# Kernel tuning notes

Measured on AMD Instinct MI355X. Metric: run time of the kernel, lower is better.

The kernel has to match this reference:

```python
import jax, jax.numpy as jnp
import numpy as np
import math

D, H, S, B, E, FF = 768, 12, 1024, 2, 32768, 4 * 768
HD = D // H


def layer_norm(x, g, b, eps=1e-5):
    m = jnp.mean(x, axis=-1, keepdims=True)
    v = jnp.mean((x - m) ** 2, axis=-1, keepdims=True)
    return (x - m) / jnp.sqrt(v + eps) * g + b


def setup_inputs() -> dict:
    key = jax.random.key(0)
    ks = jax.random.split(key, 24)
    w = lambda k, shape: jax.random.normal(k, shape, dtype=jnp.float32) * 0.02
    inp = {
        "x": jax.random.normal(ks[0], (B, S, D), dtype=jnp.float32),
        "adj_mask": jax.random.randint(ks[1], (B, S, S), 0, 2).astype(bool),
        "edge_attr": jax.random.normal(ks[2], (E,), dtype=jnp.float32),
        "edge_index": jax.random.randint(ks[3], (2, E), 0, S),
        "norm1_g": jnp.ones((D,), jnp.float32),
        "norm1_b": jnp.zeros((D,), jnp.float32),
        "Wq": w(ks[4], (D, D)), "bq": jnp.zeros((D,), jnp.float32),
        "Wk": w(ks[5], (D, D)), "bk": jnp.zeros((D,), jnp.float32),
        "Wv": w(ks[6], (D, D)), "bv": jnp.zeros((D,), jnp.float32),
        "Wo": w(ks[7], (D, D)), "bo": jnp.zeros((D,), jnp.float32),
        "norm2_g": jnp.ones((D,), jnp.float32),
        "norm2_b": jnp.zeros((D,), jnp.float32),
        "mlp_W1": w(ks[8], (D, FF)), "mlp_b1": jnp.zeros((FF,), jnp.float32),
        "mlp_W2": w(ks[9], (FF, D)), "mlp_b2": jnp.zeros((D,), jnp.float32),
        # per-head edge-attr MLP: Linear(1,16) -> GELU -> Linear(16,1), stacked over H heads
        "ep_W1": w(ks[10], (H, 16)), "ep_b1": jnp.zeros((H, 16), jnp.float32),
        "ep_W2": w(ks[11], (H, 16)), "ep_b2": jnp.zeros((H,), jnp.float32),
    }
    return inp


def reference(x, adj_mask, edge_attr, edge_index,
              norm1_g, norm1_b, Wq, bq, Wk, bk, Wv, bv, Wo, bo,
              norm2_g, norm2_b, mlp_W1, mlp_b1, mlp_W2, mlp_b2,
              ep_W1, ep_b1, ep_W2, ep_b2):
    Bb, Ss, Dd = x.shape
    Hh = ep_W1.shape[0]
    hd = Dd // Hh
    residual = x
    nx = layer_norm(x, norm1_g, norm1_b)
    q = (nx @ Wq + bq).reshape(Bb, Ss, Hh, hd).transpose(0, 2, 1, 3)  # [B,H,S,hd]
    k = (nx @ Wk + bk).reshape(Bb, Ss, Hh, hd).transpose(0, 2, 1, 3)
    v = (nx @ Wv + bv).reshape(Bb, Ss, Hh, hd).transpose(0, 2, 1, 3)
    scores = jnp.einsum('bhqd,bhkd->bhqk', q, k) / math.sqrt(hd)
    mask = adj_mask.astype(bool)[:, None]  # [B,1,S,S]
    scores = jnp.where(mask, scores, jnp.float32(-1e9))
    # per-edge per-head bias (computed under no_grad in the original -> stop_gradient)
    h1 = jax.nn.gelu(edge_attr[:, None, None] * ep_W1[None] + ep_b1[None], approximate=False)  # [E,H,16]
    proj = jnp.einsum('ehk,hk->eh', h1, ep_W2) + ep_b2  # [E,H]
    proj = jax.lax.stop_gradient(proj)
    src, dst = edge_index[0], edge_index[1]
    bias = jnp.zeros((Hh, Ss, Ss), x.dtype).at[:, src, dst].set(proj.T)  # [H,S,S]
    scores = scores + jnp.where(mask, bias[None], jnp.float32(0.0))
    attn = jax.nn.softmax(scores, axis=-1)
    out = jnp.einsum('bhqk,bhkd->bhqd', attn, v)
    out = out.transpose(0, 2, 1, 3).reshape(Bb, Ss, Dd)
    x = residual + (out @ Wo + bo)
    y = layer_norm(x, norm2_g, norm2_b)
    y = jax.nn.gelu(y @ mlp_W1 + mlp_b1, approximate=False) @ mlp_W2 + mlp_b2
    return x + y
```

## Files before the change

### kernel.cpp

```cpp
#include <hip/hip_runtime.h>
#include <hip/hip_bf16.h>

#define B_ 2
#define S_ 1024
#define D_ 768
#define H_ 12
#define HD_ 64
#define FF_ 3072
#define E_ 32768
#define QS_ 2304
#define NSPLIT 4
#define NSPLIT_W2 4
#define BHS (B_ * H_ * S_)

typedef short bf16x8 __attribute__((ext_vector_type(8)));
typedef float f32x4 __attribute__((ext_vector_type(4)));

#define SW(row, seg) ((((seg) ^ ((row) & 7)) * 8))

__device__ __forceinline__ unsigned short f2bf(float f) {
    __hip_bfloat16 h = __float2bfloat16(f);
    return __builtin_bit_cast(unsigned short, h);
}
__device__ __forceinline__ float bf2f(unsigned short u) {
    unsigned int v = ((unsigned int)u) << 16;
    return __builtin_bit_cast(float, v);
}
__device__ __forceinline__ float gelu_exact(float x) {
    return 0.5f * x * (1.0f + erff(x * 0.70710678118654752f));
}
__device__ __forceinline__ void gload_lds16(const unsigned short* g, unsigned short* l) {
    __builtin_amdgcn_global_load_lds((const __attribute__((address_space(1))) void*)g,
                                     (__attribute__((address_space(3))) void*)l, 16, 0, 0);
}

__global__ __launch_bounds__(256) void prep_kernel(
    const void* __restrict__ adj, unsigned int* __restrict__ mp, int* __restrict__ winner,
    const float* __restrict__ Wq, const float* __restrict__ Wk, const float* __restrict__ Wv,
    const float* __restrict__ Wo, const float* __restrict__ W1, const float* __restrict__ W2,
    unsigned short* __restrict__ wqkvt, unsigned short* __restrict__ wot,
    unsigned short* __restrict__ w1t, unsigned short* __restrict__ w2t,
    const float* __restrict__ bq, const float* __restrict__ bk, const float* __restrict__ bv,
    float* __restrict__ bqkv,
    const float* __restrict__ x, const float* __restrict__ g1, const float* __restrict__ bn1,
    unsigned short* __restrict__ nxb)
{
    __shared__ float tile[32][33];
    __shared__ unsigned int words[32];
    __shared__ int u8f;
    __shared__ float red[8];
    const int blk = blockIdx.x;
    const int t = threadIdx.x;

    if (blk < 2048) {
        const int b = blk >> 10, q = blk & 1023;
        if (b == 0) {
            int4 v; v.x = -1; v.y = -1; v.z = -1; v.w = -1;
            reinterpret_cast<int4*>(winner)[q * 256 + t] = v;
        }
        if (t < 32) words[t] = 0;
        if (t == 0) u8f = 0;
        __syncthreads();
        const unsigned int* row8 = (const unsigned int*)((const unsigned char*)adj + ((size_t)b * S_ + q) * S_);
        const unsigned int* row32 = (const unsigned int*)((const int*)adj + ((size_t)b * S_ + q) * S_);
        const unsigned int v = row8[t];
        if (v & 0xFF00FF00u) atomicOr(&u8f, 1);
        __syncthreads();
        if (u8f) {
            unsigned int nib = 0;
            if (v & 0x000000FFu) nib |= 1u;
            if (v & 0x0000FF00u) nib |= 2u;
            if (v & 0x00FF0000u) nib |= 4u;
            if (v & 0xFF000000u) nib |= 8u;
            if (nib) atomicOr(&words[t >> 3], nib << ((t & 7) * 4));
        } else {
            for (int i = 0; i < 4; i++) {
                const int k = i * 256 + t;
                if (row32[k]) atomicOr(&words[k >> 5], 1u << (k & 31));
            }
        }
        __syncthreads();
        if (t < 32) mp[((size_t)b * S_ + q) * 32 + t] = words[t];
    } else if (blk < 8960) {
        const int w = blk - 2048;
        const float* src; unsigned short* dst; int K, N, nb, kb;
        if (w < 2304) {
            const int z = w / 576, r = w - z * 576;
            K = 768; N = 768; kb = (r / 24) * 32; nb = (r % 24) * 32;
            src = (z == 0) ? Wq : (z == 1) ? Wk : (z == 2) ? Wv : Wo;
            dst = (z == 3) ? wot : wqkvt + (size_t)z * 768 * 768;
        } else if (w < 4608) {
            const int r = w - 2304;
            K = 768; N = 3072; nb = (r % 96) * 32; kb = (r / 96) * 32;
            src = W1; dst = w1t;
        } else {
            const int r = w - 4608;
            K = 3072; N = 768; kb = (r % 96) * 32; nb = (r / 96) * 32;
            src = W2; dst = w2t;
        }
        const int tx = t & 31, ty = t >> 5;
        for (int r = 0; r < 32; r += 8)
            tile[ty + r][tx] = src[(size_t)(kb + ty + r) * N + nb + tx];
        __syncthreads();
        for (int r = 0; r < 32; r += 8)
            dst[(size_t)(nb + ty + r) * K + kb + tx] = f2bf(tile[tx][ty + r]);
        if (w == 0) {
            for (int i = t; i < QS_; i += 256)
                bqkv[i] = (i < 768) ? bq[i] : (i < 1536) ? bk[i - 768] : bv[i - 1536];
        }
    } else {
        const int row = blk - 8960;
        const float* xr = x + (size_t)row * D_;
        float v0 = xr[t], v1 = xr[t + 256], v2 = xr[t + 512];
        float s = v0 + v1 + v2, s2 = v0 * v0 + v1 * v1 + v2 * v2;
        for (int m = 32; m; m >>= 1) { s += __shfl_xor(s, m); s2 += __shfl_xor(s2, m); }
        const int w = t >> 6;
        if ((t & 63) == 0) { red[w] = s; red[4 + w] = s2; }
        __syncthreads();
        s = red[0] + red[1] + red[2] + red[3];
        s2 = red[4] + red[5] + red[6] + red[7];
        const float mean = s * (1.f / D_);
        const float var = s2 * (1.f / D_) - mean * mean;
        const float rstd = rsqrtf(var + 1e-5f);
        unsigned short* orow = nxb + (size_t)row * D_;
        orow[t]       = f2bf((v0 - mean) * rstd * g1[t]       + bn1[t]);
        orow[t + 256] = f2bf((v1 - mean) * rstd * g1[t + 256] + bn1[t + 256]);
        orow[t + 512] = f2bf((v2 - mean) * rstd * g1[t + 512] + bn1[t + 512]);
    }
}

__global__ __launch_bounds__(256) void ln_kernel(
    const float* __restrict__ x, const float* __restrict__ g,
    const float* __restrict__ b, unsigned short* __restrict__ out)
{
    const int row = blockIdx.x;
    const int t = threadIdx.x;
    const float* xr = x + (size_t)row * D_;
    float v0 = xr[t], v1 = xr[t + 256], v2 = xr[t + 512];
    float s = v0 + v1 + v2, s2 = v0 * v0 + v1 * v1 + v2 * v2;
    for (int m = 32; m; m >>= 1) { s += __shfl_xor(s, m); s2 += __shfl_xor(s2, m); }
    __shared__ float red[8];
    const int w = t >> 6;
    if ((t & 63) == 0) { red[w] = s; red[4 + w] = s2; }
    __syncthreads();
    s = red[0] + red[1] + red[2] + red[3];
    s2 = red[4] + red[5] + red[6] + red[7];
    const float mean = s * (1.f / D_);
    const float var = s2 * (1.f / D_) - mean * mean;
    const float rstd = rsqrtf(var + 1e-5f);
    unsigned short* orow = out + (size_t)row * D_;
    orow[t]       = f2bf((v0 - mean) * rstd * g[t]       + b[t]);
    orow[t + 256] = f2bf((v1 - mean) * rstd * g[t + 256] + b[t + 256]);
    orow[t + 512] = f2bf((v2 - mean) * rstd * g[t + 512] + b[t + 512]);
}

__global__ __launch_bounds__(256) void edge_proj_scatter_kernel(
    const float* __restrict__ ea, const float* __restrict__ W1, const float* __restrict__ b1,
    const float* __restrict__ W2, const float* __restrict__ b2,
    const int* __restrict__ ei, float* __restrict__ proj, int* __restrict__ winner)
{
    const int tid = blockIdx.x * 256 + threadIdx.x;
    const int e = tid / H_, h = tid - e * H_;
    const float a = ea[e];
    float s = 0.f;
    for (int j = 0; j < 16; j++) {
        const float tv = a * W1[h * 16 + j] + b1[h * 16 + j];
        s += gelu_exact(tv) * W2[h * 16 + j];
    }
    proj[tid] = s + b2[h];
    if (h == 0) {
        const int sn = ei[e], dn = ei[E_ + e];
        atomicMax(&winner[sn * S_ + dn], e);
    }
}

__global__ __launch_bounds__(256) void mid_kernel(
    const unsigned short* __restrict__ qkv, unsigned short* __restrict__ vt,
    const int* __restrict__ winner, const float* __restrict__ proj,
    unsigned short* __restrict__ ebias)
{
    __shared__ unsigned short T[64][68];
    const int blk = blockIdx.x;
    const int t = threadIdx.x;
    if (blk < 384) {
        const int s0 = (blk & 15) * 64;
        const int rest = blk >> 4;
        const int h = rest % 12, b = rest / 12;
        const int r = t >> 2, seg = t & 3;
        const unsigned short* src = qkv + (size_t)(b * S_ + s0 + r) * QS_ + 1536 + h * HD_ + seg * 16;
        *reinterpret_cast<uint4*>(&T[r][seg * 16])     = *reinterpret_cast<const uint4*>(src);
        *reinterpret_cast<uint4*>(&T[r][seg * 16 + 8]) = *reinterpret_cast<const uint4*>(src + 8);
        __syncthreads();
        unsigned short tmp[16];
        for (int i = 0; i < 16; i++) tmp[i] = T[seg * 16 + i][r];
        unsigned short* dst = vt + ((size_t)(b * H_ + h) * HD_ + r) * S_ + s0 + seg * 16;
        *reinterpret_cast<uint4*>(dst)     = *reinterpret_cast<uint4*>(&tmp[0]);
        *reinterpret_cast<uint4*>(dst + 8) = *reinterpret_cast<uint4*>(&tmp[8]);
    } else {
        const int q = blk - 384;
        const int k4 = t * 4;
        const int4 wv = *reinterpret_cast<const int4*>(&winner[q * S_ + k4]);
        for (int h = 0; h < H_; h++) {
            unsigned int lo = 0, hi = 0;
            if (wv.x >= 0) lo |= (unsigned int)f2bf(proj[(size_t)wv.x * H_ + h]);
            if (wv.y >= 0) lo |= ((unsigned int)f2bf(proj[(size_t)wv.y * H_ + h])) << 16;
            if (wv.z >= 0) hi |= (unsigned int)f2bf(proj[(size_t)wv.z * H_ + h]);
            if (wv.w >= 0) hi |= ((unsigned int)f2bf(proj[(size_t)wv.w * H_ + h])) << 16;
            uint2 val; val.x = lo; val.y = hi;
            *reinterpret_cast<uint2*>(&ebias[((size_t)h * S_ + q) * S_ + k4]) = val;
        }
    }
}

template<bool RES, bool OUTBF>
__global__ __launch_bounds__(256) void gemm_kernel(
    const unsigned short* __restrict__ A, const unsigned short* __restrict__ Bt,
    const float* __restrict__ bias, const float* __restrict__ res,
    void* __restrict__ outp, int M, int N, int K)
{
    __shared__ unsigned short As[64][40];
    __shared__ unsigned short Bs[64][40];
    const int m0 = blockIdx.y * 64, n0 = blockIdx.x * 64;
    const int t = threadIdx.x;
    const int w = t >> 6, l = t & 63;
    const int wm = w >> 1, wn = w & 1;
    const int r = l & 15, g = l >> 4;
    const int srow = t >> 2, sseg = t & 3;
    f32x4 acc[2][2] = {};
    for (int k0 = 0; k0 < K; k0 += 32) {
        __syncthreads();
        const uint4 av = *reinterpret_cast<const uint4*>(A + (size_t)(m0 + srow) * K + k0 + sseg * 8);
        *reinterpret_cast<uint4*>(&As[srow][sseg * 8]) = av;
        const uint4 bv = *reinterpret_cast<const uint4*>(Bt + (size_t)(n0 + srow) * K + k0 + sseg * 8);
        *reinterpret_cast<uint4*>(&Bs[srow][sseg * 8]) = bv;
        __syncthreads();
        bf16x8 af[2], bfr[2];
        af[0]  = *reinterpret_cast<const bf16x8*>(&As[wm * 32 + r][g * 8]);
        af[1]  = *reinterpret_cast<const bf16x8*>(&As[wm * 32 + 16 + r][g * 8]);
        bfr[0] = *reinterpret_cast<const bf16x8*>(&Bs[wn * 32 + r][g * 8]);
        bfr[1] = *reinterpret_cast<const bf16x8*>(&Bs[wn * 32 + 16 + r][g * 8]);
        for (int m = 0; m < 2; m++)
            for (int n = 0; n < 2; n++)
                acc[m][n] = __builtin_amdgcn_mfma_f32_16x16x32_bf16(af[m], bfr[n], acc[m][n], 0, 0, 0);
    }
    for (int m = 0; m < 2; m++)
        for (int n = 0; n < 2; n++) {
            const int col = n0 + wn * 32 + n * 16 + r;
            const float bvv = bias[col];
            for (int j = 0; j < 4; j++) {
                const int row = m0 + wm * 32 + m * 16 + g * 4 + j;
                float v = acc[m][n][j] + bvv;
                if (RES) v += res[(size_t)row * N + col];
                if (OUTBF) ((unsigned short*)outp)[(size_t)row * N + col] = f2bf(v);
                else       ((float*)outp)[(size_t)row * N + col] = v;
            }
        }
}

template<bool GELU, bool OUTBF, bool SPLITK>
__global__ __launch_bounds__(256) void gemm128_kernel(
    const unsigned short* __restrict__ A, const unsigned short* __restrict__ Bt,
    const float* __restrict__ bias, void* __restrict__ outp,
    int M, int N, int K, int klen, int scale_below)
{
    __shared__ unsigned short As[128][64];
    __shared__ unsigned short Bs[128][64];
    const int m0 = blockIdx.y * 128, n0 = blockIdx.x * 128;
    const int t = threadIdx.x;
    const int w = t >> 6, l = t & 63;
    const int wm = w >> 1, wn = w & 1;
    const int lr = l & 15, g = l >> 4;
    const int lrow8 = l >> 3;
    const int lseg = (l & 7) ^ lrow8;
    const int kbeg = SPLITK ? blockIdx.z * klen : 0;
    const int kend = SPLITK ? kbeg + klen : K;
    f32x4 acc[4][4] = {};
    for (int k0 = kbeg; k0 < kend; k0 += 64) {
        __syncthreads();
        for (int j = 0; j < 4; j++) {
            const int q = w * 4 + j;
            const int row = q * 8 + lrow8;
            gload_lds16(A  + (size_t)(m0 + row) * K + k0 + lseg * 8, &As[q * 8][0]);
            gload_lds16(Bt + (size_t)(n0 + row) * K + k0 + lseg * 8, &Bs[q * 8][0]);
        }
        __syncthreads();
        for (int kk = 0; kk < 2; kk++) {
            bf16x8 af[4], bfr[4];
            for (int m = 0; m < 4; m++) {
                const int r = wm * 64 + m * 16 + lr;
                af[m] = *reinterpret_cast<const bf16x8*>(&As[r][SW(r, kk * 4 + g)]);
            }
            for (int n = 0; n < 4; n++) {
                const int r = wn * 64 + n * 16 + lr;
                bfr[n] = *reinterpret_cast<const bf16x8*>(&Bs[r][SW(r, kk * 4 + g)]);
            }
            for (int m = 0; m < 4; m++)
                for (int n = 0; n < 4; n++)
                    acc[m][n] = __builtin_amdgcn_mfma_f32_16x16x32_bf16(af[m], bfr[n], acc[m][n], 0, 0, 0);
        }
    }
    if (SPLITK) {
        for (int m = 0; m < 4; m++)
            for (int n = 0; n < 4; n++) {
                const int col = n0 + wn * 64 + n * 16 + lr;
                for (int j = 0; j < 4; j++) {
                    const int row = m0 + wm * 64 + m * 16 + g * 4 + j;
                    if (OUTBF) ((unsigned short*)outp)[((size_t)blockIdx.z * M + row) * N + col] = f2bf(acc[m][n][j]);
                    else       ((float*)outp)[((size_t)blockIdx.z * M + row) * N + col] = acc[m][n][j];
                }
            }
    } else {
        for (int m = 0; m < 4; m++)
            for (int n = 0; n < 4; n++) {
                const int col = n0 + wn * 64 + n * 16 + lr;
                const float scl = (col < scale_below) ? 0.125f : 1.0f;
                const float bvv = bias[col];
                for (int j = 0; j < 4; j++) {
                    const int row = m0 + wm * 64 + m * 16 + g * 4 + j;
                    float v = (acc[m][n][j] + bvv) * scl;
                    if (GELU) v = gelu_exact(v);
                    if (OUTBF) ((unsigned short*)outp)[(size_t)row * N + col] = f2bf(v);
                    else       ((float*)outp)[(size_t)row * N + col] = v;
                }
            }
    }
}

__global__ __launch_bounds__(256) void w2_reduce_kernel(
    const unsigned short* __restrict__ part, const float* __restrict__ x2,
    const float* __restrict__ b2, float* __restrict__ out)
{
    const int idx = (blockIdx.x * 256 + threadIdx.x) * 4;
    const int col = idx % D_;
    const float4 xr = *reinterpret_cast<const float4*>(&x2[idx]);
    const float4 bb = *reinterpret_cast<const float4*>(&b2[col]);
    float4 o;
    o.x = xr.x + bb.x; o.y = xr.y + bb.y; o.z = xr.z + bb.z; o.w = xr.w + bb.w;
    for (int s = 0; s < NSPLIT_W2; s++) {
        const uint2 p = *reinterpret_cast<const uint2*>(&part[(size_t)s * B_ * S_ * D_ + idx]);
        o.x += bf2f((unsigned short)(p.x & 0xFFFF));
        o.y += bf2f((unsigned short)(p.x >> 16));
        o.z += bf2f((unsigned short)(p.y & 0xFFFF));
        o.w += bf2f((unsigned short)(p.y >> 16));
    }
    *reinterpret_cast<float4*>(&out[idx]) = o;
}

__global__ __launch_bounds__(256) void attn_mfma_kernel(
    const unsigned short* __restrict__ qkv,
    const unsigned short* __restrict__ vt,
    const unsigned short* __restrict__ ebias,
    const unsigned int* __restrict__ mp,
    unsigned short* __restrict__ pacc,
    float2* __restrict__ pml)
{
    __shared__ unsigned short Ks[64][64];
    __shared__ unsigned short Vs[64][64];
    __shared__ unsigned short Eb[64][72];
    __shared__ unsigned int   Mw[64][2];
    __shared__ unsigned short Ps[4][16][64];
    const int t = threadIdx.x;
    const int w = t >> 6, l = t & 63;
    const int lr = l & 15, g = l >> 4;
    const int qt = blockIdx.x & 15, sp = blockIdx.x >> 4;
    const int q0 = qt * 64;
    const int h = blockIdx.y, b = blockIdx.z;
    const int bh = b * H_ + h;
    const size_t qbase = (size_t)b * S_ * QS_ + h * HD_;
    const size_t kbase = qbase + 768;
    const size_t vtbase = (size_t)bh * HD_ * S_;

    const int qrow = q0 + w * 16 + lr;
    const bf16x8 af0 = *reinterpret_cast<const bf16x8*>(qkv + qbase + (size_t)qrow * QS_ + g * 8);
    const bf16x8 af1 = *reinterpret_cast<const bf16x8*>(qkv + qbase + (size_t)qrow * QS_ + 32 + g * 8);

    float m_run[4], l_run[4];
    f32x4 acc[4] = {};
    for (int j = 0; j < 4; j++) { m_run[j] = -3.0e38f; l_run[j] = 0.f; }

    const int srow = t >> 2, sseg = t & 3;
    const int kt_beg = sp * (S_ / NSPLIT), kt_end = kt_beg + S_ / NSPLIT;
    for (int kt = kt_beg; kt < kt_end; kt += 64) {
        __syncthreads();
        {
            const unsigned short* ksrc = qkv + kbase + (size_t)(kt + srow) * QS_ + sseg * 16;
            *reinterpret_cast<uint4*>(&Ks[srow][SW(srow, sseg * 2)])     = *reinterpret_cast<const uint4*>(ksrc);
            *reinterpret_cast<uint4*>(&Ks[srow][SW(srow, sseg * 2 + 1)]) = *reinterpret_cast<const uint4*>(ksrc + 8);
            const unsigned short* vsrc = vt + vtbase + (size_t)srow * S_ + kt + sseg * 16;
            *reinterpret_cast<uint4*>(&Vs[srow][SW(srow, sseg * 2)])     = *reinterpret_cast<const uint4*>(vsrc);
            *reinterpret_cast<uint4*>(&Vs[srow][SW(srow, sseg * 2 + 1)]) = *reinterpret_cast<const uint4*>(vsrc + 8);
            const unsigned short* esrc = ebias + ((size_t)h * S_ + q0 + srow) * S_ + kt + sseg * 16;
            *reinterpret_cast<uint4*>(&Eb[srow][sseg * 16])     = *reinterpret_cast<const uint4*>(esrc);
            *reinterpret_cast<uint4*>(&Eb[srow][sseg * 16 + 8]) = *reinterpret_cast<const uint4*>(esrc + 8);
            if (t < 128) Mw[t >> 1][t & 1] = mp[((size_t)b * S_ + q0 + (t >> 1)) * 32 + (kt >> 5) + (t & 1)];
        }
        __syncthreads();
        f32x4 sc[4];
        for (int n = 0; n < 4; n++) {
            const int r = n * 16 + lr;
            const bf16x8 b0 = *reinterpret_cast<const bf16x8*>(&Ks[r][SW(r, g)]);
            const bf16x8 b1 = *reinterpret_cast<const bf16x8*>(&Ks[r][SW(r, 4 + g)]);
            f32x4 z = {};
            z = __builtin_amdgcn_mfma_f32_16x16x32_bf16(af0, b0, z, 0, 0, 0);
            z = __builtin_amdgcn_mfma_f32_16x16x32_bf16(af1, b1, z, 0, 0, 0);
            sc[n] = z;
        }
        float tmax[4] = {-3.0e38f, -3.0e38f, -3.0e38f, -3.0e38f};
        for (int n = 0; n < 4; n++) {
            for (int j = 0; j < 4; j++) {
                const int rq = w * 16 + g * 4 + j;
                const unsigned int word = Mw[rq][n >> 1];
                const bool msk = (word >> ((n & 1) * 16 + lr)) & 1;
                float sval;
                if (msk) sval = sc[n][j] + bf2f(Eb[rq][n * 16 + lr]);
                else sval = -1e9f;
                sc[n][j] = sval;
                tmax[j] = fmaxf(tmax[j], sval);
            }
        }
        float pscale[4];
        for (int j = 0; j < 4; j++) {
            float tm = tmax[j];
            tm = fmaxf(tm, __shfl_xor(tm, 1));
            tm = fmaxf(tm, __shfl_xor(tm, 2));
            tm = fmaxf(tm, __shfl_xor(tm, 4));
            tm = fmaxf(tm, __shfl_xor(tm, 8));
            const float mnew = fmaxf(m_run[j], tm);
            pscale[j] = __expf(m_run[j] - mnew);
            m_run[j] = mnew;
            l_run[j] *= pscale[j];
        }
        float psum[4] = {0.f, 0.f, 0.f, 0.f};
        for (int n = 0; n < 4; n++) {
            for (int j = 0; j < 4; j++) {
                const float p = __expf(sc[n][j] - m_run[j]);
                psum[j] += p;
                const int row = g * 4 + j;
                Ps[w][row][SW(row, n * 2 + (lr >> 3)) + (lr & 7)] = f2bf(p);
            }
        }
        for (int j = 0; j < 4; j++) {
            float s = psum[j];
            s += __shfl_xor(s, 1); s += __shfl_xor(s, 2);
            s += __shfl_xor(s, 4); s += __shfl_xor(s, 8);
            l_run[j] += s;
            for (int n2 = 0; n2 < 4; n2++) acc[n2][j] *= pscale[j];
        }
        const bf16x8 pa0 = *reinterpret_cast<const bf16x8*>(&Ps[w][lr][SW(lr, g)]);
        const bf16x8 pa1 = *reinterpret_cast<const bf16x8*>(&Ps[w][lr][SW(lr, 4 + g)]);
        for (int n2 = 0; n2 < 4; n2++) {
            const int r = n2 * 16 + lr;
            const bf16x8 vb0 = *reinterpret_cast<const bf16x8*>(&Vs[r][SW(r, g)]);
            const bf16x8 vb1 = *reinterpret_cast<const bf16x8*>(&Vs[r][SW(r, 4 + g)]);
            acc[n2] = __builtin_amdgcn_mfma_f32_16x16x32_bf16(pa0, vb0, acc[n2], 0, 0, 0);
            acc[n2] = __builtin_amdgcn_mfma_f32_16x16x32_bf16(pa1, vb1, acc[n2], 0, 0, 0);
        }
    }
    const size_t prow = (size_t)sp * BHS + (size_t)bh * S_;
    for (int j = 0; j < 4; j++) {
        const int qg = q0 + w * 16 + g * 4 + j;
        for (int n2 = 0; n2 < 4; n2++)
            pacc[(prow + qg) * 64 + n2 * 16 + lr] = f2bf(acc[n2][j]);
        if (lr == 0) { float2 v; v.x = m_run[j]; v.y = l_run[j]; pml[prow + qg] = v; }
    }
}

__global__ __launch_bounds__(256) void attn_combine_kernel(
    const unsigned short* __restrict__ pacc, const float2* __restrict__ pml,
    unsigned short* __restrict__ attnb)
{
    const int idx = (blockIdx.x * 256 + threadIdx.x) * 4;
    const int r = idx >> 6, d = idx & 63;
    float2 ml[NSPLIT];
    float mx = -3.0e38f;
    for (int s = 0; s < NSPLIT; s++) {
        ml[s] = pml[(size_t)s * BHS + r];
        mx = fmaxf(mx, ml[s].x);
    }
    float wgt[NSPLIT], L = 0.f;
    for (int s = 0; s < NSPLIT; s++) {
        wgt[s] = __expf(ml[s].x - mx);
        L += ml[s].y * wgt[s];
    }
    const float inv = (L > 0.f) ? 1.f / L : 0.f;
    float4 o = {0.f, 0.f, 0.f, 0.f};
    for (int s = 0; s < NSPLIT; s++) {
        const uint2 p = *reinterpret_cast<const uint2*>(&pacc[((size_t)s * BHS + r) * 64 + d]);
        o.x += bf2f((unsigned short)(p.x & 0xFFFF)) * wgt[s];
        o.y += bf2f((unsigned short)(p.x >> 16)) * wgt[s];
        o.z += bf2f((unsigned short)(p.y & 0xFFFF)) * wgt[s];
        o.w += bf2f((unsigned short)(p.y >> 16)) * wgt[s];
    }
    const int bh = r >> 10, q = r & 1023;
    const int b = bh / H_, h = bh - b * H_;
    ushort4 ov;
    ov.x = f2bf(o.x * inv); ov.y = f2bf(o.y * inv);
    ov.z = f2bf(o.z * inv); ov.w = f2bf(o.w * inv);
    *reinterpret_cast<ushort4*>(&attnb[((size_t)(b * S_ + q)) * D_ + h * HD_ + d]) = ov;
}

extern "C" void kernel_launch(void* const* d_in, const int* in_sizes, int n_in,
                              void* d_out, int out_size, void* d_ws, size_t ws_size,
                              hipStream_t stream)
{
    const float* x    = (const float*)d_in[0];
    const void*  adj  = d_in[1];
    const float* ea   = (const float*)d_in[2];
    const int*   ei   = (const int*)d_in[3];
    const float* g1   = (const float*)d_in[4];
    const float* bn1  = (const float*)d_in[5];
    const float* Wq   = (const float*)d_in[6];
    const float* bq   = (const float*)d_in[7];
    const float* Wk   = (const float*)d_in[8];
    const float* bk   = (const float*)d_in[9];
    const float* Wv   = (const float*)d_in[10];
    const float* bv   = (const float*)d_in[11];
    const float* Wo   = (const float*)d_in[12];
    const float* bo   = (const float*)d_in[13];
    const float* g2   = (const float*)d_in[14];
    const float* bn2  = (const float*)d_in[15];
    const float* W1   = (const float*)d_in[16];
    const float* mb1  = (const float*)d_in[17];
    const float* W2   = (const float*)d_in[18];
    const float* mb2  = (const float*)d_in[19];
    const float* epW1 = (const float*)d_in[20];
    const float* epb1 = (const float*)d_in[21];
    const float* epW2 = (const float*)d_in[22];
    const float* epb2 = (const float*)d_in[23];

    char* ws = (char*)d_ws;
    size_t off = 0;
    auto carve = [&](size_t bytes) -> void* {
        void* p = ws + off;
        off += (bytes + 255) & ~(size_t)255;
        return p;
    };
    unsigned short* wqkvt = (unsigned short*)carve((size_t)QS_ * D_ * 2);
    unsigned short* wot   = (unsigned short*)carve((size_t)D_ * D_ * 2);
    unsigned short* w1t   = (unsigned short*)carve((size_t)FF_ * D_ * 2);
    unsigned short* w2t   = (unsigned short*)carve((size_t)D_ * FF_ * 2);
    float*          bqkv  = (float*)carve((size_t)QS_ * 4);
    float*          proj  = (float*)carve((size_t)E_ * H_ * 4);
    int*            winner= (int*)carve((size_t)S_ * S_ * 4);
    unsigned short* ebias = (unsigned short*)carve((size_t)H_ * S_ * S_ * 2);
    unsigned int*   mpk   = (unsigned int*)carve((size_t)B_ * S_ * 32 * 4);
    unsigned short* nxb   = (unsigned short*)carve((size_t)B_ * S_ * D_ * 2);
    unsigned short* attnb = (unsigned short*)carve((size_t)B_ * S_ * D_ * 2);
    unsigned short* qkv   = (unsigned short*)carve((size_t)B_ * S_ * QS_ * 2);
    unsigned short* vtb   = (unsigned short*)carve((size_t)B_ * S_ * D_ * 2);
    float*          x2f   = (float*)carve((size_t)B_ * S_ * D_ * 4);
    unsigned short* pacc  = (unsigned short*)carve((size_t)NSPLIT * BHS * 64 * 2);
    float2*         pml   = (float2*)carve((size_t)NSPLIT * BHS * 8);
    unsigned short* ln2b = nxb;
    unsigned short* hb   = qkv;
    unsigned short* pw2  = (unsigned short*)ebias;

    const int M = B_ * S_;

    prep_kernel<<<11008, 256, 0, stream>>>(
        adj, mpk, winner,
        Wq, Wk, Wv, Wo, W1, W2, wqkvt, wot, w1t, w2t, bq, bk, bv, bqkv,
        x, g1, bn1, nxb);

    edge_proj_scatter_kernel<<<(E_ * H_) / 256, 256, 0, stream>>>(
        ea, epW1, epb1, epW2, epb2, ei, proj, winner);

    gemm128_kernel<false, true, false><<<dim3(QS_ / 128, M / 128), 256, 0, stream>>>(
        nxb, wqkvt, bqkv, qkv, M, QS_, D_, D_, 768);

    mid_kernel<<<384 + S_, 256, 0, stream>>>(qkv, vtb, winner, proj, ebias);

    attn_mfma_kernel<<<dim3(16 * NSPLIT, H_, B_), 256, 0, stream>>>(
        qkv, vtb, ebias, mpk, pacc, pml);
    attn_combine_kernel<<<(BHS * 64) / 1024, 256, 0, stream>>>(pacc, pml, attnb);

    gemm_kernel<true, false><<<dim3(D_ / 64, M / 64), 256, 0, stream>>>(
        attnb, wot, bo, x, x2f, M, D_, D_);

    ln_kernel<<<M, 256, 0, stream>>>(x2f, g2, bn2, ln2b);

    gemm128_kernel<true, true, false><<<dim3(FF_ / 128, M / 128), 256, 0, stream>>>(
        ln2b, w1t, mb1, hb, M, FF_, D_, D_, 0);
    gemm128_kernel<false, true, true><<<dim3(D_ / 128, M / 128, NSPLIT_W2), 256, 0, stream>>>(
        hb, w2t, mb2, pw2, M, D_, FF_, FF_ / NSPLIT_W2, 0);
    w2_reduce_kernel<<<(M * D_) / 1024, 256, 0, stream>>>(pw2, x2f, mb2, (float*)d_out);
}
```

Baseline: 182.3 us.

## Fuse QKV GEMM with V-transpose and edge-bias fill; share edge bias across batches

Replaces the separate QKV GEMM and mid kernel with one kernel. Half its grid runs a 128x128 MFMA GEMM whose epilogue writes V directly in transposed layout. The other half expands the edge-bias matrix from the winner and projection arrays. The attention kernel now handles both batch elements per block, so each edge-bias tile is loaded once and reused for both batches instead of being fetched twice. The cost is halved attention grid parallelism, doubled register and LDS use per block, and scalar strided qkv stores in the GEMM epilogue.

```diff
diff --git a/kernel.cpp b/kernel.cpp
--- a/kernel.cpp
+++ b/kernel.cpp
@@ -174,41 +174,94 @@
     }
 }
 
-__global__ __launch_bounds__(256) void mid_kernel(
-    const unsigned short* __restrict__ qkv, unsigned short* __restrict__ vt,
+__global__ __launch_bounds__(256) void qkv_kernel(
+    const unsigned short* __restrict__ A, const unsigned short* __restrict__ Bt,
+    const float* __restrict__ bias, unsigned short* __restrict__ qkv,
+    unsigned short* __restrict__ vt,
     const int* __restrict__ winner, const float* __restrict__ proj,
     unsigned short* __restrict__ ebias)
 {
-    __shared__ unsigned short T[64][68];
-    const int blk = blockIdx.x;
+    if (blockIdx.z == 1) {
+        const int id = blockIdx.y * 18 + blockIdx.x;
+        const int t = threadIdx.x;
+        const int k4 = t * 4;
+        for (int r = 0; r < 4; r++) {
+            const int q = id * 4 + r;
+            if (q >= S_) return;
+            const int4 wv = *reinterpret_cast<const int4*>(&winner[q * S_ + k4]);
+            for (int h = 0; h < H_; h++) {
+                unsigned int lo = 0, hi = 0;
+                if (wv.x >= 0) lo |= (unsigned int)f2bf(proj[(size_t)wv.x * H_ + h]);
+                if (wv.y >= 0) lo |= ((unsigned int)f2bf(proj[(size_t)wv.y * H_ + h])) << 16;
+                if (wv.z >= 0) hi |= (unsigned int)f2bf(proj[(size_t)wv.z * H_ + h]);
+                if (wv.w >= 0) hi |= ((unsigned int)f2bf(proj[(size_t)wv.w * H_ + h])) << 16;
+                uint2 val; val.x = lo; val.y = hi;
+                *reinterpret_cast<uint2*>(&ebias[((size_t)h * S_ + q) * S_ + k4]) = val;
+            }
+        }
+        return;
+    }
+    __shared__ unsigned short As[128][64];
+    __shared__ unsigned short Bs[128][64];
+    const int m0 = blockIdx.y * 128, n0 = blockIdx.x * 128;
     const int t = threadIdx.x;
-    if (blk < 384) {
-        const int s0 = (blk & 15) * 64;
-        const int rest = blk >> 4;
-        const int h = rest % 12, b = rest / 12;
-        const int r = t >> 2, seg = t & 3;
-        const unsigned short* src = qkv + (size_t)(b * S_ + s0 + r) * QS_ + 1536 + h * HD_ + seg * 16;
-        *reinterpret_cast<uint4*>(&T[r][seg * 16])     = *reinterpret_cast<const uint4*>(src);
-        *reinterpret_cast<uint4*>(&T[r][seg * 16 + 8]) = *reinterpret_cast<const uint4*>(src + 8);
-        __syncthreads();
-        unsigned short tmp[16];
-        for (int i = 0; i < 16; i++) tmp[i] = T[seg * 16 + i][r];
-        unsigned short* dst = vt + ((size_t)(b * H_ + h) * HD_ + r) * S_ + s0 + seg * 16;
-        *reinterpret_cast<uint4*>(dst)     = *reinterpret_cast<uint4*>(&tmp[0]);
-        *reinterpret_cast<uint4*>(dst + 8) = *reinterpret_cast<uint4*>(&tmp[8]);
+    const int w = t >> 6, l = t & 63;
+    const int wm = w >> 1, wn = w & 1;
+    const int lr = l & 15, g = l >> 4;
+    const int lrow8 = l >> 3;
+    const int lseg = (l & 7) ^ lrow8;
+    f32x4 acc[4][4] = {};
+    for (int k0 = 0; k0 < D_; k0 += 64) {
+        __syncthreads();
+        for (int j = 0; j < 4; j++) {
+            const int q = w * 4 + j;
+            const int row = q * 8 + lrow8;
+            gload_lds16(A  + (size_t)(m0 + row) * D_ + k0 + lseg * 8, &As[q * 8][0]);
+            gload_lds16(Bt + (size_t)(n0 + row) * D_ + k0 + lseg * 8, &Bs[q * 8][0]);
+        }
+        __syncthreads();
+        for (int kk = 0; kk < 2; kk++) {
+            bf16x8 af[4], bfr[4];
+            for (int m = 0; m < 4; m++) {
+                const int r = wm * 64 + m * 16 + lr;
+                af[m] = *reinterpret_cast<const bf16x8*>(&As[r][SW(r, kk * 4 + g)]);
+            }
+            for (int n = 0; n < 4; n++) {
+                const int r = wn * 64 + n * 16 + lr;
+                bfr[n] = *reinterpret_cast<const bf16x8*>(&Bs[r][SW(r, kk * 4 + g)]);
+            }
+            for (int m = 0; m < 4; m++)
+                for (int n = 0; n < 4; n++)
+                    acc[m][n] = __builtin_amdgcn_mfma_f32_16x16x32_bf16(af[m], bfr[n], acc[m][n], 0, 0, 0);
+        }
+    }
+    if (n0 >= 1536) {
+        for (int m = 0; m < 4; m++)
+            for (int n = 0; n < 4; n++) {
+                const int col = n0 + wn * 64 + n * 16 + lr;
+                const int vcol = col - 1536;
+                const int hh = vcol >> 6, d = vcol & 63;
+                const float bvv = bias[col];
+                const int grow = m0 + wm * 64 + m * 16 + g * 4;
+                const int bb = grow >> 10, s = grow & 1023;
+                ushort4 o;
+                o.x = f2bf(acc[m][n][0] + bvv);
+                o.y = f2bf(acc[m][n][1] + bvv);
+                o.z = f2bf(acc[m][n][2] + bvv);
+                o.w = f2bf(acc[m][n][3] + bvv);
+                *reinterpret_cast<ushort4*>(&vt[(((size_t)(bb * H_ + hh) * HD_) + d) * S_ + s]) = o;
+            }
     } else {
-        const int q = blk - 384;
-        const int k4 = t * 4;
-        const int4 wv = *reinterpret_cast<const int4*>(&winner[q * S_ + k4]);
-        for (int h = 0; h < H_; h++) {
-            unsigned int lo = 0, hi = 0;
-            if (wv.x >= 0) lo |= (unsigned int)f2bf(proj[(size_t)wv.x * H_ + h]);
-            if (wv.y >= 0) lo |= ((unsigned int)f2bf(proj[(size_t)wv.y * H_ + h])) << 16;
-            if (wv.z >= 0) hi |= (unsigned int)f2bf(proj[(size_t)wv.z * H_ + h]);
-            if (wv.w >= 0) hi |= ((unsigned int)f2bf(proj[(size_t)wv.w * H_ + h])) << 16;
-            uint2 val; val.x = lo; val.y = hi;
-            *reinterpret_cast<uint2*>(&ebias[((size_t)h * S_ + q) * S_ + k4]) = val;
-        }
+        for (int m = 0; m < 4; m++)
+            for (int n = 0; n < 4; n++) {
+                const int col = n0 + wn * 64 + n * 16 + lr;
+                const float scl = (col < 768) ? 0.125f : 1.0f;
+                const float bvv = bias[col];
+                for (int j = 0; j < 4; j++) {
+                    const int row = m0 + wm * 64 + m * 16 + g * 4 + j;
+                    qkv[(size_t)row * QS_ + col] = f2bf((acc[m][n][j] + bvv) * scl);
+                }
+            }
     }
 }
 
@@ -354,114 +407,126 @@
     unsigned short* __restrict__ pacc,
     float2* __restrict__ pml)
 {
-    __shared__ unsigned short Ks[64][64];
-    __shared__ unsigned short Vs[64][64];
+    __shared__ unsigned short Ks[2][64][64];
+    __shared__ unsigned short Vs[2][64][64];
     __shared__ unsigned short Eb[64][72];
-    __shared__ unsigned int   Mw[64][2];
+    __shared__ unsigned int   Mw[2][64][2];
     __shared__ unsigned short Ps[4][16][64];
     const int t = threadIdx.x;
     const int w = t >> 6, l = t & 63;
     const int lr = l & 15, g = l >> 4;
     const int qt = blockIdx.x & 15, sp = blockIdx.x >> 4;
     const int q0 = qt * 64;
-    const int h = blockIdx.y, b = blockIdx.z;
-    const int bh = b * H_ + h;
-    const size_t qbase = (size_t)b * S_ * QS_ + h * HD_;
-    const size_t kbase = qbase + 768;
-    const size_t vtbase = (size_t)bh * HD_ * S_;
-
-    const int qrow = q0 + w * 16 + lr;
-    const bf16x8 af0 = *reinterpret_cast<const bf16x8*>(qkv + qbase + (size_t)qrow * QS_ + g * 8);
-    const bf16x8 af1 = *reinterpret_cast<const bf16x8*>(qkv + qbase + (size_t)qrow * QS_ + 32 + g * 8);
-
-    float m_run[4], l_run[4];
-    f32x4 acc[4] = {};
-    for (int j = 0; j < 4; j++) { m_run[j] = -3.0e38f; l_run[j] = 0.f; }
+    const int h = blockIdx.y;
+
+    bf16x8 af[2][2];
+    #pragma unroll
+    for (int bb = 0; bb < 2; bb++) {
+        const size_t qbase = (size_t)bb * S_ * QS_ + h * HD_;
+        const int qrow = q0 + w * 16 + lr;
+        af[bb][0] = *reinterpret_cast<const bf16x8*>(qkv + qbase + (size_t)qrow * QS_ + g * 8);
+        af[bb][1] = *reinterpret_cast<const bf16x8*>(qkv + qbase + (size_t)qrow * QS_ + 32 + g * 8);
+    }
+    float m_run[2][4], l_run[2][4];
+    f32x4 acc[2][4] = {};
+    #pragma unroll
+    for (int bb = 0; bb < 2; bb++)
+        for (int j = 0; j < 4; j++) { m_run[bb][j] = -3.0e38f; l_run[bb][j] = 0.f; }
 
     const int srow = t >> 2, sseg = t & 3;
     const int kt_beg = sp * (S_ / NSPLIT), kt_end = kt_beg + S_ / NSPLIT;
     for (int kt = kt_beg; kt < kt_end; kt += 64) {
         __syncthreads();
+        #pragma unroll
+        for (int bb = 0; bb < 2; bb++) {
+            const unsigned short* ksrc = qkv + (size_t)bb * S_ * QS_ + h * HD_ + 768 + (size_t)(kt + srow) * QS_ + sseg * 16;
+            *reinterpret_cast<uint4*>(&Ks[bb][srow][SW(srow, sseg * 2)])     = *reinterpret_cast<const uint4*>(ksrc);
+            *reinterpret_cast<uint4*>(&Ks[bb][srow][SW(srow, sseg * 2 + 1)]) = *reinterpret_cast<const uint4*>(ksrc + 8);
+            const unsigned short* vsrc = vt + ((size_t)(bb * H_ + h) * HD_ + srow) * S_ + kt + sseg * 16;
+            *reinterpret_cast<uint4*>(&Vs[bb][srow][SW(srow, sseg * 2)])     = *reinterpret_cast<const uint4*>(vsrc);
+            *reinterpret_cast<uint4*>(&Vs[bb][srow][SW(srow, sseg * 2 + 1)]) = *reinterpret_cast<const uint4*>(vsrc + 8);
+        }
         {
-            const unsigned short* ksrc = qkv + kbase + (size_t)(kt + srow) * QS_ + sseg * 16;
-            *reinterpret_cast<uint4*>(&Ks[srow][SW(srow, sseg * 2)])     = *reinterpret_cast<const uint4*>(ksrc);
-            *reinterpret_cast<uint4*>(&Ks[srow][SW(srow, sseg * 2 + 1)]) = *reinterpret_cast<const uint4*>(ksrc + 8);
-            const unsigned short* vsrc = vt + vtbase + (size_t)srow * S_ + kt + sseg * 16;
-            *reinterpret_cast<uint4*>(&Vs[srow][SW(srow, sseg * 2)])     = *reinterpret_cast<const uint4*>(vsrc);
-            *reinterpret_cast<uint4*>(&Vs[srow][SW(srow, sseg * 2 + 1)]) = *reinterpret_cast<const uint4*>(vsrc + 8);
             const unsigned short* esrc = ebias + ((size_t)h * S_ + q0 + srow) * S_ + kt + sseg * 16;
             *reinterpret_cast<uint4*>(&Eb[srow][sseg * 16])     = *reinterpret_cast<const uint4*>(esrc);
             *reinterpret_cast<uint4*>(&Eb[srow][sseg * 16 + 8]) = *reinterpret_cast<const uint4*>(esrc + 8);
-            if (t < 128) Mw[t >> 1][t & 1] = mp[((size_t)b * S_ + q0 + (t >> 1)) * 32 + (kt >> 5) + (t & 1)];
-        }
-        __syncthreads();
-        f32x4 sc[4];
-        for (int n = 0; n < 4; n++) {
-            const int r = n * 16 + lr;
-            const bf16x8 b0 = *reinterpret_cast<const bf16x8*>(&Ks[r][SW(r, g)]);
-            const bf16x8 b1 = *reinterpret_cast<const bf16x8*>(&Ks[r][SW(r, 4 + g)]);
-            f32x4 z = {};
-            z = __builtin_amdgcn_mfma_f32_16x16x32_bf16(af0, b0, z, 0, 0, 0);
-            z = __builtin_amdgcn_mfma_f32_16x16x32_bf16(af1, b1, z, 0, 0, 0);
-            sc[n] = z;
-        }
-        float tmax[4] = {-3.0e38f, -3.0e38f, -3.0e38f, -3.0e38f};
-        for (int n = 0; n < 4; n++) {
+            Mw[t >> 7][(t >> 1) & 63][t & 1] =
+                mp[((size_t)(t >> 7) * S_ + q0 + ((t >> 1) & 63)) * 32 + (kt >> 5) + (t & 1)];
+        }
+        __syncthreads();
+        #pragma unroll
+        for (int bb = 0; bb < 2; bb++) {
+            f32x4 sc[4];
+            for (int n = 0; n < 4; n++) {
+                const int r = n * 16 + lr;
+                const bf16x8 b0 = *reinterpret_cast<const bf16x8*>(&Ks[bb][r][SW(r, g)]);
+                const bf16x8 b1 = *reinterpret_cast<const bf16x8*>(&Ks[bb][r][SW(r, 4 + g)]);
+                f32x4 z = {};
+                z = __builtin_amdgcn_mfma_f32_16x16x32_bf16(af[bb][0], b0, z, 0, 0, 0);
+                z = __builtin_amdgcn_mfma_f32_16x16x32_bf16(af[bb][1], b1, z, 0, 0, 0);
+                sc[n] = z;
+            }
+            float tmax[4] = {-3.0e38f, -3.0e38f, -3.0e38f, -3.0e38f};
+            for (int n = 0; n < 4; n++) {
+                for (int j = 0; j < 4; j++) {
+                    const int rq = w * 16 + g * 4 + j;
+                    const unsigned int word = Mw[bb][rq][n >> 1];
+                    const bool msk = (word >> ((n & 1) * 16 + lr)) & 1;
+                    float sval;
+                    if (msk) sval = sc[n][j] + bf2f(Eb[rq][n * 16 + lr]);
+                    else sval = -1e9f;
+                    sc[n][j] = sval;
+                    tmax[j] = fmaxf(tmax[j], sval);
+                }
+            }
+            float pscale[4];
             for (int j = 0; j < 4; j++) {
-                const int rq = w * 16 + g * 4 + j;
-                const unsigned int word = Mw[rq][n >> 1];
-                const bool msk = (word >> ((n & 1) * 16 + lr)) & 1;
-                float sval;
-                if (msk) sval = sc[n][j] + bf2f(Eb[rq][n * 16 + lr]);
-                else sval = -1e9f;
-                sc[n][j] = sval;
-                tmax[j] = fmaxf(tmax[j], sval);
-            }
-        }
-        float pscale[4];
+                float tm = tmax[j];
+                tm = fmaxf(tm, __shfl_xor(tm, 1));
+                tm = fmaxf(tm, __shfl_xor(tm, 2));
+                tm = fmaxf(tm, __shfl_xor(tm, 4));
+                tm = fmaxf(tm, __shfl_xor(tm, 8));
+                const float mnew = fmaxf(m_run[bb][j], tm);
+                pscale[j] = __expf(m_run[bb][j] - mnew);
+                m_run[bb][j] = mnew;
+                l_run[bb][j] *= pscale[j];
+            }
+            float psum[4] = {0.f, 0.f, 0.f, 0.f};
+            for (int n = 0; n < 4; n++) {
+                for (int j = 0; j < 4; j++) {
+                    const float p = __expf(sc[n][j] - m_run[bb][j]);
+                    psum[j] += p;
+                    const int row = g * 4 + j;
+                    Ps[w][row][SW(row, n * 2 + (lr >> 3)) + (lr & 7)] = f2bf(p);
+                }
+            }
+            for (int j = 0; j < 4; j++) {
+                float s = psum[j];
+                s += __shfl_xor(s, 1); s += __shfl_xor(s, 2);
+                s += __shfl_xor(s, 4); s += __shfl_xor(s, 8);
+                l_run[bb][j] += s;
+                for (int n2 = 0; n2 < 4; n2++) acc[bb][n2][j] *= pscale[j];
+            }
+            const bf16x8 pa0 = *reinterpret_cast<const bf16x8*>(&Ps[w][lr][SW(lr, g)]);
+            const bf16x8 pa1 = *reinterpret_cast<const bf16x8*>(&Ps[w][lr][SW(lr, 4 + g)]);
+            for (int n2 = 0; n2 < 4; n2++) {
+                const int r = n2 * 16 + lr;
+                const bf16x8 vb0 = *reinterpret_cast<const bf16x8*>(&Vs[bb][r][SW(r, g)]);
+                const bf16x8 vb1 = *reinterpret_cast<const bf16x8*>(&Vs[bb][r][SW(r, 4 + g)]);
+                acc[bb][n2] = __builtin_amdgcn_mfma_f32_16x16x32_bf16(pa0, vb0, acc[bb][n2], 0, 0, 0);
+                acc[bb][n2] = __builtin_amdgcn_mfma_f32_16x16x32_bf16(pa1, vb1, acc[bb][n2], 0, 0, 0);
+            }
+        }
+    }
+    #pragma unroll
+    for (int bb = 0; bb < 2; bb++) {
+        const size_t prow = (size_t)sp * BHS + (size_t)(bb * H_ + h) * S_;
         for (int j = 0; j < 4; j++) {
-            float tm = tmax[j];
-            tm = fmaxf(tm, __shfl_xor(tm, 1));
-            tm = fmaxf(tm, __shfl_xor(tm, 2));
-            tm = fmaxf(tm, __shfl_xor(tm, 4));
-            tm = fmaxf(tm, __shfl_xor(tm, 8));
-            const float mnew = fmaxf(m_run[j], tm);
-            pscale[j] = __expf(m_run[j] - mnew);
-            m_run[j] = mnew;
-            l_run[j] *= pscale[j];
-        }
-        float psum[4] = {0.f, 0.f, 0.f, 0.f};
-        for (int n = 0; n < 4; n++) {
-            for (int j = 0; j < 4; j++) {
-                const float p = __expf(sc[n][j] - m_run[j]);
-                psum[j] += p;
-                const int row = g * 4 + j;
-                Ps[w][row][SW(row, n * 2 + (lr >> 3)) + (lr & 7)] = f2bf(p);
-            }
-        }
-        for (int j = 0; j < 4; j++) {
-            float s = psum[j];
-            s += __shfl_xor(s, 1); s += __shfl_xor(s, 2);
-            s += __shfl_xor(s, 4); s += __shfl_xor(s, 8);
-            l_run[j] += s;
-            for (int n2 = 0; n2 < 4; n2++) acc[n2][j] *= pscale[j];
-        }
-        const bf16x8 pa0 = *reinterpret_cast<const bf16x8*>(&Ps[w][lr][SW(lr, g)]);
-        const bf16x8 pa1 = *reinterpret_cast<const bf16x8*>(&Ps[w][lr][SW(lr, 4 + g)]);
-        for (int n2 = 0; n2 < 4; n2++) {
-            const int r = n2 * 16 + lr;
-            const bf16x8 vb0 = *reinterpret_cast<const bf16x8*>(&Vs[r][SW(r, g)]);
-            const bf16x8 vb1 = *reinterpret_cast<const bf16x8*>(&Vs[r][SW(r, 4 + g)]);
-            acc[n2] = __builtin_amdgcn_mfma_f32_16x16x32_bf16(pa0, vb0, acc[n2], 0, 0, 0);
-            acc[n2] = __builtin_amdgcn_mfma_f32_16x16x32_bf16(pa1, vb1, acc[n2], 0, 0, 0);
-        }
-    }
-    const size_t prow = (size_t)sp * BHS + (size_t)bh * S_;
-    for (int j = 0; j < 4; j++) {
-        const int qg = q0 + w * 16 + g * 4 + j;
-        for (int n2 = 0; n2 < 4; n2++)
-            pacc[(prow + qg) * 64 + n2 * 16 + lr] = f2bf(acc[n2][j]);
-        if (lr == 0) { float2 v; v.x = m_run[j]; v.y = l_run[j]; pml[prow + qg] = v; }
+            const int qg = q0 + w * 16 + g * 4 + j;
+            for (int n2 = 0; n2 < 4; n2++)
+                pacc[(prow + qg) * 64 + n2 * 16 + lr] = f2bf(acc[bb][n2][j]);
+            if (lr == 0) { float2 v; v.x = m_run[bb][j]; v.y = l_run[bb][j]; pml[prow + qg] = v; }
+        }
     }
 }
 
@@ -565,12 +630,10 @@
     edge_proj_scatter_kernel<<<(E_ * H_) / 256, 256, 0, stream>>>(
         ea, epW1, epb1, epW2, epb2, ei, proj, winner);
 
-    gemm128_kernel<false, true, false><<<dim3(QS_ / 128, M / 128), 256, 0, stream>>>(
-        nxb, wqkvt, bqkv, qkv, M, QS_, D_, D_, 768);
-
-    mid_kernel<<<384 + S_, 256, 0, stream>>>(qkv, vtb, winner, proj, ebias);
-
-    attn_mfma_kernel<<<dim3(16 * NSPLIT, H_, B_), 256, 0, stream>>>(
+    qkv_kernel<<<dim3(QS_ / 128, M / 128, 2), 256, 0, stream>>>(
+        nxb, wqkvt, bqkv, qkv, vtb, winner, proj, ebias);
+
+    attn_mfma_kernel<<<dim3(16 * NSPLIT, H_), 256, 0, stream>>>(
         qkv, vtb, ebias, mpk, pacc, pml);
     attn_combine_kernel<<<(BHS * 64) / 1024, 256, 0, stream>>>(pacc, pml, attnb);
 
```

After: 222.5 us. 22.1% more time.
